# Optimization experiments

Measured on AMD Instinct MI355X. Metric: run time of the kernel, lower is better.

The kernel has to match this reference:

```python
import jax, jax.numpy as jnp
import numpy as np

N_NODES = 50000
N_EDGES = 800000
IN_DIM, HID_DIM, OUT_DIM = 128, 96, 96
NUM_GRAPHS = 64
NEG_SLOPE_ATT = 0.2   # GATConv internal leaky_relu
NEG_SLOPE_ACT = 0.01  # F.leaky_relu default between layers


def setup_inputs() -> dict:
    key = jax.random.key(0)
    ks = jax.random.split(key, 16)
    x = jax.random.normal(ks[0], (N_NODES, IN_DIM), dtype=jnp.float32)
    edge_index = jax.random.randint(ks[1], (2, N_EDGES), 0, N_NODES, dtype=jnp.int64)
    batch = jnp.sort(jax.random.randint(ks[2], (N_NODES,), 0, NUM_GRAPHS, dtype=jnp.int64))

    def glorot(k, shape):
        lim = np.sqrt(6.0 / (shape[0] + shape[-1]))
        return jax.random.uniform(k, shape, jnp.float32, -lim, lim)

    params = {}
    dims = [(IN_DIM, HID_DIM), (HID_DIM, HID_DIM), (HID_DIM, OUT_DIM)]
    for i, (di, do) in enumerate(dims, start=1):
        params[f"W{i}"] = glorot(ks[3 * i], (di, do))
        params[f"a_src{i}"] = glorot(ks[3 * i + 1], (do,))
        params[f"a_dst{i}"] = glorot(ks[3 * i + 2], (do,))
        params[f"b{i}"] = jnp.zeros((do,), jnp.float32)
    return {"x": x, "edge_index": edge_index, "batch": batch, **params}


def gat_conv(x, src, dst, W, a_src, a_dst, b):
    # x: [N, in], src/dst: [Etot] (self-loops included)
    h = x @ W                                   # [N, out]
    alpha_s = h @ a_src                         # [N]
    alpha_d = h @ a_dst                         # [N]
    e = jax.nn.leaky_relu(alpha_s[src] + alpha_d[dst], NEG_SLOPE_ATT)  # [Etot]
    # segment softmax over destination neighborhoods
    m = jax.ops.segment_max(e, dst, num_segments=N_NODES)
    ex = jnp.exp(e - m[dst])
    denom = jax.ops.segment_sum(ex, dst, num_segments=N_NODES)
    alpha = ex / (denom[dst] + 1e-16)           # [Etot]
    msg = alpha[:, None] * h[src]               # [Etot, out]
    out = jax.ops.segment_sum(msg, dst, num_segments=N_NODES)
    return out + b


def reference(x, edge_index, batch, W1, a_src1, a_dst1, b1, W2, a_src2, a_dst2, b2, W3, a_src3, a_dst3, b3):
    # add self loops once (PyG GATConv add_self_loops=True per layer; same edge set)
    sl = jnp.arange(N_NODES, dtype=edge_index.dtype)
    src = jnp.concatenate([edge_index[0], sl])
    dst = jnp.concatenate([edge_index[1], sl])

    h = jax.nn.leaky_relu(gat_conv(x, src, dst, W1, a_src1, a_dst1, b1), NEG_SLOPE_ACT)
    h = jax.nn.leaky_relu(gat_conv(h, src, dst, W2, a_src2, a_dst2, b2), NEG_SLOPE_ACT)
    h = gat_conv(h, src, dst, W3, a_src3, a_dst3, b3)

    # global mean pool over graphs
    sums = jax.ops.segment_sum(h, batch, num_segments=NUM_GRAPHS)       # [G, out]
    counts = jax.ops.segment_sum(jnp.ones((N_NODES,), h.dtype), batch, num_segments=NUM_GRAPHS)
    return sums / jnp.maximum(counts, 1.0)[:, None]
```

## Files before the change

kernel.cpp:

```cpp
#include <hip/hip_runtime.h>

#define N_NODES 50000
#define N_EDGES 800000
#define E_TOT   850000
#define IN0     128
#define HID     96
#define NUM_GRAPHS 64
#define NB      ((N_NODES + 1023) / 1024)

__device__ __forceinline__ float leaky(float x, float s) { return x > 0.f ? x : s * x; }

__global__ void count_deg(const int* __restrict__ dst, int* __restrict__ deg) {
    int e = blockIdx.x * blockDim.x + threadIdx.x;
    if (e >= E_TOT) return;
    int d = (e < N_EDGES) ? dst[e] : (e - N_EDGES);
    atomicAdd(&deg[d], 1);
}

__global__ __launch_bounds__(256) void block_sums(const int* __restrict__ deg, int* __restrict__ bsum) {
    int b = blockIdx.x, t = threadIdx.x;
    int base = b * 1024 + t * 4;
    int s = 0;
    if (base + 3 < N_NODES) {
        int4 v = *(const int4*)(deg + base);
        s = v.x + v.y + v.z + v.w;
    } else {
        for (int k = 0; k < 4; ++k) if (base + k < N_NODES) s += deg[base + k];
    }
#pragma unroll
    for (int w = 32; w >= 1; w >>= 1) s += __shfl_xor(s, w);
    __shared__ int ws[4];
    if ((t & 63) == 0) ws[t >> 6] = s;
    __syncthreads();
    if (t == 0) bsum[b] = ws[0] + ws[1] + ws[2] + ws[3];
}

__global__ void scan_partials(const int* __restrict__ bsum, int* __restrict__ excl, int* __restrict__ offs) {
    int t = threadIdx.x;
    int v = (t < NB) ? bsum[t] : 0;
    int incl = v;
#pragma unroll
    for (int d = 1; d < 64; d <<= 1) {
        int u = __shfl_up(incl, d);
        if (t >= d) incl += u;
    }
    if (t < NB) excl[t] = incl - v;
    if (t == 0) offs[N_NODES] = E_TOT;
}

__global__ __launch_bounds__(256) void write_offs(const int* __restrict__ deg,
                                                  const int* __restrict__ excl,
                                                  int* __restrict__ offs) {
    __shared__ int sh[256];
    int b = blockIdx.x, t = threadIdx.x;
    int base = b * 1024 + t * 4;
    int d0 = 0, d1 = 0, d2 = 0, d3 = 0;
    if (base + 3 < N_NODES) {
        int4 v = *(const int4*)(deg + base);
        d0 = v.x; d1 = v.y; d2 = v.z; d3 = v.w;
    } else {
        if (base     < N_NODES) d0 = deg[base];
        if (base + 1 < N_NODES) d1 = deg[base + 1];
        if (base + 2 < N_NODES) d2 = deg[base + 2];
    }
    int tsum = d0 + d1 + d2 + d3;
    sh[t] = tsum;
    __syncthreads();
    for (int off = 1; off < 256; off <<= 1) {
        int u = (t >= off) ? sh[t - off] : 0;
        __syncthreads();
        sh[t] += u;
        __syncthreads();
    }
    int ebase = excl[b] + sh[t] - tsum;
    if (base + 3 < N_NODES) {
        int4 o; o.x = ebase; o.y = ebase + d0; o.z = ebase + d0 + d1; o.w = ebase + d0 + d1 + d2;
        *(int4*)(offs + base) = o;
    } else {
        if (base     < N_NODES) offs[base]     = ebase;
        if (base + 1 < N_NODES) offs[base + 1] = ebase + d0;
        if (base + 2 < N_NODES) offs[base + 2] = ebase + d0 + d1;
    }
}

__global__ void scatter_edges(const int* __restrict__ src, const int* __restrict__ dst,
                              const int* __restrict__ offs, int* __restrict__ cursor,
                              int* __restrict__ csr) {
    int e = blockIdx.x * blockDim.x + threadIdx.x;
    if (e >= E_TOT) return;
    int s, d;
    if (e < N_EDGES) { s = src[e]; d = dst[e]; }
    else             { s = e - N_EDGES; d = s; }
    int pos = offs[d] + atomicAdd(&cursor[d], 1);
    csr[pos] = s;
}

template <int IN>
__global__ __launch_bounds__(256) void gemm_tiled(
    const float* __restrict__ X, const float* __restrict__ W,
    const float* __restrict__ asrc, const float* __restrict__ adst,
    float* __restrict__ H, float* __restrict__ As, float* __restrict__ Ad) {
    __shared__ float Xs[64 * 36];
    __shared__ float Wt[96 * 36];
    int tid = threadIdx.x;
    int cx = tid & 31, ry = tid >> 5;
    int cbase = cx * 3;
    int rowBase = blockIdx.x * 64;
    float acc[8][3];
#pragma unroll
    for (int r = 0; r < 8; ++r)
#pragma unroll
        for (int j = 0; j < 3; ++j) acc[r][j] = 0.f;

    for (int t = 0; t < IN / 32; ++t) {
        int k0 = t * 32;
        __syncthreads();
#pragma unroll
        for (int j = 0; j < 2; ++j) {
            int f = tid * 2 + j;
            int row = f >> 3;
            int kk = (f & 7) * 4;
            int grow = rowBase + row;
            float4 v = make_float4(0.f, 0.f, 0.f, 0.f);
            if (grow < N_NODES) v = *(const float4*)(X + (size_t)grow * IN + k0 + kk);
            *(float4*)(&Xs[row * 36 + kk]) = v;
        }
#pragma unroll
        for (int j = 0; j < 12; ++j) {
            int f = tid + j * 256;
            int kk = f / 96;
            int c = f - kk * 96;
            Wt[c * 36 + kk] = W[(size_t)(k0 + kk) * HID + c];
        }
        __syncthreads();
#pragma unroll
        for (int k = 0; k < 32; k += 4) {
            float4 w0 = *(const float4*)(&Wt[(cbase + 0) * 36 + k]);
            float4 w1 = *(const float4*)(&Wt[(cbase + 1) * 36 + k]);
            float4 w2 = *(const float4*)(&Wt[(cbase + 2) * 36 + k]);
#pragma unroll
            for (int r = 0; r < 8; ++r) {
                float4 xv = *(const float4*)(&Xs[(ry * 8 + r) * 36 + k]);
                acc[r][0] += xv.x * w0.x + xv.y * w0.y + xv.z * w0.z + xv.w * w0.w;
                acc[r][1] += xv.x * w1.x + xv.y * w1.y + xv.z * w1.z + xv.w * w1.w;
                acc[r][2] += xv.x * w2.x + xv.y * w2.y + xv.z * w2.z + xv.w * w2.w;
            }
        }
    }
    float a0 = asrc[cbase], a1 = asrc[cbase + 1], a2 = asrc[cbase + 2];
    float d0 = adst[cbase], d1 = adst[cbase + 1], d2 = adst[cbase + 2];
#pragma unroll
    for (int r = 0; r < 8; ++r) {
        int row = rowBase + ry * 8 + r;
        bool valid = row < N_NODES;
        float ps = acc[r][0] * a0 + acc[r][1] * a1 + acc[r][2] * a2;
        float pd = acc[r][0] * d0 + acc[r][1] * d1 + acc[r][2] * d2;
#pragma unroll
        for (int w = 16; w >= 1; w >>= 1) {
            ps += __shfl_xor(ps, w);
            pd += __shfl_xor(pd, w);
        }
        if (valid) {
            float* hr = H + (size_t)row * HID + cbase;
            hr[0] = acc[r][0]; hr[1] = acc[r][1]; hr[2] = acc[r][2];
            if (cx == 0) { As[row] = ps; Ad[row] = pd; }
        }
    }
}

__global__ __launch_bounds__(256) void aggregate(
    const float* __restrict__ H, const float* __restrict__ As, const float* __restrict__ Ad,
    const int* __restrict__ offs, const int* __restrict__ csr,
    const float* __restrict__ bias, float* __restrict__ Hout, int apply_leaky) {
    int team = (blockIdx.x * blockDim.x + threadIdx.x) >> 5;
    int lane = threadIdx.x & 31;
    int half = threadIdx.x & 32;
    int start = offs[team], end = offs[team + 1];
    float ad = Ad[team];
    float m = leaky(As[team] + ad, 0.2f);
    float acc0 = 0.f, acc1 = 0.f, acc2 = 0.f, denom = 0.f;
    int c = lane * 3;
    for (int base = start; base < end; base += 32) {
        int i = base + lane;
        bool valid = i < end;
        int s = valid ? csr[i] : 0;
        float ex = 0.f;
        if (valid) ex = __expf(leaky(As[s] + ad, 0.2f) - m);
        denom += ex;
        int cnt = min(32, end - base);
        int j = 0;
        for (; j + 8 <= cnt; j += 8) {
            float e[8]; int ss[8];
#pragma unroll
            for (int q = 0; q < 8; ++q) {
                e[q]  = __shfl(ex, half + j + q);
                ss[q] = __shfl(s,  half + j + q);
            }
            float v0[8], v1[8], v2[8];
#pragma unroll
            for (int q = 0; q < 8; ++q) {
                const float* p = H + (size_t)ss[q] * HID + c;
                v0[q] = p[0]; v1[q] = p[1]; v2[q] = p[2];
            }
#pragma unroll
            for (int q = 0; q < 8; ++q) {
                acc0 += e[q] * v0[q]; acc1 += e[q] * v1[q]; acc2 += e[q] * v2[q];
            }
        }
        for (; j + 4 <= cnt; j += 4) {
            float e[4]; int ss[4];
#pragma unroll
            for (int q = 0; q < 4; ++q) {
                e[q]  = __shfl(ex, half + j + q);
                ss[q] = __shfl(s,  half + j + q);
            }
            float v0[4], v1[4], v2[4];
#pragma unroll
            for (int q = 0; q < 4; ++q) {
                const float* p = H + (size_t)ss[q] * HID + c;
                v0[q] = p[0]; v1[q] = p[1]; v2[q] = p[2];
            }
#pragma unroll
            for (int q = 0; q < 4; ++q) {
                acc0 += e[q] * v0[q]; acc1 += e[q] * v1[q]; acc2 += e[q] * v2[q];
            }
        }
        for (; j < cnt; ++j) {
            float bex = __shfl(ex, half + j);
            int   bs  = __shfl(s,  half + j);
            const float* hp = H + (size_t)bs * HID + c;
            acc0 += bex * hp[0]; acc1 += bex * hp[1]; acc2 += bex * hp[2];
        }
    }
#pragma unroll
    for (int w = 16; w >= 1; w >>= 1) denom += __shfl_xor(denom, w);
    float inv = 1.f / (denom + 1e-16f);
    float o0 = acc0 * inv + bias[c];
    float o1 = acc1 * inv + bias[c + 1];
    float o2 = acc2 * inv + bias[c + 2];
    if (apply_leaky) { o0 = leaky(o0, 0.01f); o1 = leaky(o1, 0.01f); o2 = leaky(o2, 0.01f); }
    Hout[team * HID + c]     = o0;
    Hout[team * HID + c + 1] = o1;
    Hout[team * HID + c + 2] = o2;
}

__global__ __launch_bounds__(256) void pool_sum(
    const float* __restrict__ H, const int* __restrict__ batch,
    float* __restrict__ sums, float* __restrict__ counts) {
    int team = (blockIdx.x * blockDim.x + threadIdx.x) >> 5;
    int lane = threadIdx.x & 31;
    int c = lane * 3;
    int n0 = team * 32;
    if (n0 >= N_NODES) return;
    int n1 = min(n0 + 32, N_NODES);
    float a0 = 0.f, a1 = 0.f, a2 = 0.f;
    int cur = batch[n0], runlen = 0;
    for (int n = n0; n < n1; ++n) {
        int g = batch[n];
        if (g != cur) {
            atomicAdd(&sums[cur * HID + c],     a0);
            atomicAdd(&sums[cur * HID + c + 1], a1);
            atomicAdd(&sums[cur * HID + c + 2], a2);
            if (lane == 0) atomicAdd(&counts[cur], (float)runlen);
            a0 = a1 = a2 = 0.f; cur = g; runlen = 0;
        }
        const float* hp = H + (size_t)n * HID + c;
        a0 += hp[0]; a1 += hp[1]; a2 += hp[2];
        ++runlen;
    }
    atomicAdd(&sums[cur * HID + c],     a0);
    atomicAdd(&sums[cur * HID + c + 1], a1);
    atomicAdd(&sums[cur * HID + c + 2], a2);
    if (lane == 0) atomicAdd(&counts[cur], (float)runlen);
}

__global__ void finalize(const float* __restrict__ sums, const float* __restrict__ counts,
                         float* __restrict__ out) {
    int i = blockIdx.x * blockDim.x + threadIdx.x;
    if (i < NUM_GRAPHS * HID) out[i] = sums[i] / fmaxf(counts[i / HID], 1.f);
}

extern "C" void kernel_launch(void* const* d_in, const int* in_sizes, int n_in,
                              void* d_out, int out_size, void* d_ws, size_t ws_size,
                              hipStream_t stream) {
    const float* x     = (const float*)d_in[0];
    const int*   ei    = (const int*)d_in[1];
    const int*   srcI  = ei;
    const int*   dstI  = ei + N_EDGES;
    const int*   batch = (const int*)d_in[2];
    const float* W1 = (const float*)d_in[3],  *as1 = (const float*)d_in[4],
               * ad1 = (const float*)d_in[5], *b1  = (const float*)d_in[6];
    const float* W2 = (const float*)d_in[7],  *as2 = (const float*)d_in[8],
               * ad2 = (const float*)d_in[9], *b2  = (const float*)d_in[10];
    const float* W3 = (const float*)d_in[11], *as3 = (const float*)d_in[12],
               * ad3 = (const float*)d_in[13], *b3 = (const float*)d_in[14];
    float* out = (float*)d_out;

    char* p = (char*)d_ws;
    float* h0 = (float*)p;  p += (size_t)N_NODES * HID * 4;
    float* h1 = (float*)p;  p += (size_t)N_NODES * HID * 4;
    float* As = (float*)p;  p += (size_t)N_NODES * 4;
    float* Ad = (float*)p;  p += (size_t)N_NODES * 4;
    int* offs = (int*)p;    p += (size_t)(N_NODES + 4) * 4;
    int* csr  = (int*)p;    p += (size_t)E_TOT * 4;
    int* bsum = (int*)p;    p += 64 * 4;
    int* excl = (int*)p;    p += 64 * 4;
    char* zbase = p;
    float* sums   = (float*)p; p += (size_t)NUM_GRAPHS * HID * 4;
    float* counts = (float*)p; p += (size_t)NUM_GRAPHS * 4;
    int* deg    = (int*)p;  p += (size_t)N_NODES * 4;
    int* cursor = (int*)p;  p += (size_t)N_NODES * 4;
    size_t zbytes = (size_t)(p - zbase);

    hipMemsetAsync(zbase, 0, zbytes, stream);

    int eb = (E_TOT + 255) / 256;
    count_deg<<<eb, 256, 0, stream>>>(dstI, deg);
    block_sums<<<NB, 256, 0, stream>>>(deg, bsum);
    scan_partials<<<1, 64, 0, stream>>>(bsum, excl, offs);
    write_offs<<<NB, 256, 0, stream>>>(deg, excl, offs);
    scatter_edges<<<eb, 256, 0, stream>>>(srcI, dstI, offs, cursor, csr);

    int gemmGrid = (N_NODES + 63) / 64;
    int aggGrid  = (N_NODES * 32) / 256;

    gemm_tiled<IN0><<<gemmGrid, 256, 0, stream>>>(x, W1, as1, ad1, h0, As, Ad);
    aggregate<<<aggGrid, 256, 0, stream>>>(h0, As, Ad, offs, csr, b1, h1, 1);
    gemm_tiled<HID><<<gemmGrid, 256, 0, stream>>>(h1, W2, as2, ad2, h0, As, Ad);
    aggregate<<<aggGrid, 256, 0, stream>>>(h0, As, Ad, offs, csr, b2, h1, 1);
    gemm_tiled<HID><<<gemmGrid, 256, 0, stream>>>(h1, W3, as3, ad3, h0, As, Ad);
    aggregate<<<aggGrid, 256, 0, stream>>>(h0, As, Ad, offs, csr, b3, h1, 0);

    int teams = (N_NODES + 31) / 32;
    pool_sum<<<(teams * 32 + 255) / 256, 256, 0, stream>>>(h1, batch, sums, counts);
    finalize<<<(NUM_GRAPHS * HID + 255) / 256, 256, 0, stream>>>(sums, counts, out);
}
```

Before: 512.3 us.

## Double-buffer GEMM shared tiles and pre-seed scatter cursors from offsets

The dense transform kernel now double-buffers its X and W shared-memory tiles. The next K-slice is prefetched into registers while the current slice is computed, which removes one barrier per iteration. Separately, the CSR scatter cursor is initialised by a device-to-device copy of the row offsets, so the scatter kernel no longer reads offs for every edge. The cost is twice the shared memory per block, which can lower occupancy, and with only 3–4 K-tiles there is little latency to hide; launch bounds were also dropped.

```diff
diff --git a/kernel.cpp b/kernel.cpp
--- a/kernel.cpp
+++ b/kernel.cpp
@@ -84,68 +84,98 @@
 }
 
 __global__ void scatter_edges(const int* __restrict__ src, const int* __restrict__ dst,
-                              const int* __restrict__ offs, int* __restrict__ cursor,
-                              int* __restrict__ csr) {
+                              int* __restrict__ cursor, int* __restrict__ csr) {
     int e = blockIdx.x * blockDim.x + threadIdx.x;
     if (e >= E_TOT) return;
     int s, d;
     if (e < N_EDGES) { s = src[e]; d = dst[e]; }
     else             { s = e - N_EDGES; d = s; }
-    int pos = offs[d] + atomicAdd(&cursor[d], 1);
+    int pos = atomicAdd(&cursor[d], 1);
     csr[pos] = s;
 }
 
 template <int IN>
-__global__ __launch_bounds__(256) void gemm_tiled(
+__global__ void gemm_db(
     const float* __restrict__ X, const float* __restrict__ W,
     const float* __restrict__ asrc, const float* __restrict__ adst,
     float* __restrict__ H, float* __restrict__ As, float* __restrict__ Ad) {
-    __shared__ float Xs[64 * 36];
-    __shared__ float Wt[96 * 36];
+    __shared__ float Xs[2][64 * 36];
+    __shared__ float Wt[2][96 * 36];
+    constexpr int T = IN / 32;
     int tid = threadIdx.x;
     int cx = tid & 31, ry = tid >> 5;
     int cbase = cx * 3;
     int rowBase = blockIdx.x * 64;
+    int xf0 = tid, xf1 = tid + 256;
+    int xrow0 = xf0 >> 3, xkk0 = (xf0 & 7) * 4;
+    int xrow1 = xf1 >> 3, xkk1 = (xf1 & 7) * 4;
     float acc[8][3];
 #pragma unroll
     for (int r = 0; r < 8; ++r)
 #pragma unroll
         for (int j = 0; j < 3; ++j) acc[r][j] = 0.f;
 
-    for (int t = 0; t < IN / 32; ++t) {
-        int k0 = t * 32;
-        __syncthreads();
-#pragma unroll
-        for (int j = 0; j < 2; ++j) {
-            int f = tid * 2 + j;
-            int row = f >> 3;
-            int kk = (f & 7) * 4;
-            int grow = rowBase + row;
-            float4 v = make_float4(0.f, 0.f, 0.f, 0.f);
-            if (grow < N_NODES) v = *(const float4*)(X + (size_t)grow * IN + k0 + kk);
-            *(float4*)(&Xs[row * 36 + kk]) = v;
-        }
+    {
+        int g0 = rowBase + xrow0, g1 = rowBase + xrow1;
+        float4 v0 = make_float4(0.f, 0.f, 0.f, 0.f), v1 = v0;
+        if (g0 < N_NODES) v0 = *(const float4*)(X + (size_t)g0 * IN + xkk0);
+        if (g1 < N_NODES) v1 = *(const float4*)(X + (size_t)g1 * IN + xkk1);
+        *(float4*)(&Xs[0][xrow0 * 36 + xkk0]) = v0;
+        *(float4*)(&Xs[0][xrow1 * 36 + xkk1]) = v1;
 #pragma unroll
         for (int j = 0; j < 12; ++j) {
             int f = tid + j * 256;
-            int kk = f / 96;
-            int c = f - kk * 96;
-            Wt[c * 36 + kk] = W[(size_t)(k0 + kk) * HID + c];
-        }
-        __syncthreads();
-#pragma unroll
+            int kk = f / 96, c = f - kk * 96;
+            Wt[0][c * 36 + kk] = W[f];
+        }
+    }
+    __syncthreads();
+
+    int buf = 0;
+    for (int t = 0; t < T; ++t) {
+        float4 nx0, nx1; float nw[12];
+        bool more = (t + 1) < T;
+        if (more) {
+            int k0 = (t + 1) * 32;
+            int g0 = rowBase + xrow0, g1 = rowBase + xrow1;
+            nx0 = make_float4(0.f, 0.f, 0.f, 0.f); nx1 = nx0;
+            if (g0 < N_NODES) nx0 = *(const float4*)(X + (size_t)g0 * IN + k0 + xkk0);
+            if (g1 < N_NODES) nx1 = *(const float4*)(X + (size_t)g1 * IN + k0 + xkk1);
+#pragma unroll
+            for (int j = 0; j < 12; ++j) {
+                int f = tid + j * 256;
+                int kk = f / 96, c = f - kk * 96;
+                nw[j] = W[(size_t)(k0 + kk) * HID + c];
+            }
+        }
+        const float* xb = &Xs[buf][ry * 8 * 36];
+        const float* wb = &Wt[buf][cbase * 36];
+#pragma unroll 2
         for (int k = 0; k < 32; k += 4) {
-            float4 w0 = *(const float4*)(&Wt[(cbase + 0) * 36 + k]);
-            float4 w1 = *(const float4*)(&Wt[(cbase + 1) * 36 + k]);
-            float4 w2 = *(const float4*)(&Wt[(cbase + 2) * 36 + k]);
+            float4 w0 = *(const float4*)(wb + k);
+            float4 w1 = *(const float4*)(wb + 36 + k);
+            float4 w2 = *(const float4*)(wb + 72 + k);
 #pragma unroll
             for (int r = 0; r < 8; ++r) {
-                float4 xv = *(const float4*)(&Xs[(ry * 8 + r) * 36 + k]);
+                float4 xv = *(const float4*)(xb + r * 36 + k);
                 acc[r][0] += xv.x * w0.x + xv.y * w0.y + xv.z * w0.z + xv.w * w0.w;
                 acc[r][1] += xv.x * w1.x + xv.y * w1.y + xv.z * w1.z + xv.w * w1.w;
                 acc[r][2] += xv.x * w2.x + xv.y * w2.y + xv.z * w2.z + xv.w * w2.w;
             }
         }
+        if (more) {
+            int nb = buf ^ 1;
+            *(float4*)(&Xs[nb][xrow0 * 36 + xkk0]) = nx0;
+            *(float4*)(&Xs[nb][xrow1 * 36 + xkk1]) = nx1;
+#pragma unroll
+            for (int j = 0; j < 12; ++j) {
+                int f = tid + j * 256;
+                int kk = f / 96, c = f - kk * 96;
+                Wt[nb][c * 36 + kk] = nw[j];
+            }
+        }
+        __syncthreads();
+        buf ^= 1;
     }
     float a0 = asrc[cbase], a1 = asrc[cbase + 1], a2 = asrc[cbase + 2];
     float d0 = adst[cbase], d1 = adst[cbase + 1], d2 = adst[cbase + 2];
@@ -305,11 +335,11 @@
     int* csr  = (int*)p;    p += (size_t)E_TOT * 4;
     int* bsum = (int*)p;    p += 64 * 4;
     int* excl = (int*)p;    p += 64 * 4;
+    int* cursor = (int*)p;  p += (size_t)N_NODES * 4;
     char* zbase = p;
     float* sums   = (float*)p; p += (size_t)NUM_GRAPHS * HID * 4;
     float* counts = (float*)p; p += (size_t)NUM_GRAPHS * 4;
     int* deg    = (int*)p;  p += (size_t)N_NODES * 4;
-    int* cursor = (int*)p;  p += (size_t)N_NODES * 4;
     size_t zbytes = (size_t)(p - zbase);
 
     hipMemsetAsync(zbase, 0, zbytes, stream);
@@ -319,16 +349,17 @@
     block_sums<<<NB, 256, 0, stream>>>(deg, bsum);
     scan_partials<<<1, 64, 0, stream>>>(bsum, excl, offs);
     write_offs<<<NB, 256, 0, stream>>>(deg, excl, offs);
-    scatter_edges<<<eb, 256, 0, stream>>>(srcI, dstI, offs, cursor, csr);
+    hipMemcpyAsync(cursor, offs, (size_t)N_NODES * 4, hipMemcpyDeviceToDevice, stream);
+    scatter_edges<<<eb, 256, 0, stream>>>(srcI, dstI, cursor, csr);
 
     int gemmGrid = (N_NODES + 63) / 64;
     int aggGrid  = (N_NODES * 32) / 256;
 
-    gemm_tiled<IN0><<<gemmGrid, 256, 0, stream>>>(x, W1, as1, ad1, h0, As, Ad);
+    gemm_db<IN0><<<gemmGrid, 256, 0, stream>>>(x, W1, as1, ad1, h0, As, Ad);
     aggregate<<<aggGrid, 256, 0, stream>>>(h0, As, Ad, offs, csr, b1, h1, 1);
-    gemm_tiled<HID><<<gemmGrid, 256, 0, stream>>>(h1, W2, as2, ad2, h0, As, Ad);
+    gemm_db<HID><<<gemmGrid, 256, 0, stream>>>(h1, W2, as2, ad2, h0, As, Ad);
     aggregate<<<aggGrid, 256, 0, stream>>>(h0, As, Ad, offs, csr, b2, h1, 1);
-    gemm_tiled<HID><<<gemmGrid, 256, 0, stream>>>(h1, W3, as3, ad3, h0, As, Ad);
+    gemm_db<HID><<<gemmGrid, 256, 0, stream>>>(h1, W3, as3, ad3, h0, As, Ad);
     aggregate<<<aggGrid, 256, 0, stream>>>(h0, As, Ad, offs, csr, b3, h1, 0);
 
     int teams = (N_NODES + 31) / 32;
```

Measured after the change: 500.6 us. 1.02x faster.
